# Kernel tuning notes

Hardware: AMD Instinct MI355X
Metric: run time of the kernel (lower is better)

Reference implementation:

```python
import jax, jax.numpy as jnp
import numpy as np

DIM = 256; HEADS = 8; DEPTH = 2; DFF = 128
T = 64      # timesteps (transformer batch dim for s_transformer)
N = 2048    # total agents
S = 256     # number of segments (scenes)
L = 8       # agents per segment (N = S*L)
HD = DIM // HEADS
LN_EPS = 1e-5


def _ln(x, w, b):
    m = x.mean(-1, keepdims=True)
    v = x.var(-1, keepdims=True)
    return (x - m) / jnp.sqrt(v + LN_EPS) * w + b


def _mha(x, qkvw, qkvb, ow, ob):
    B, Sq, D = x.shape
    qkv = x @ qkvw.T + qkvb                      # [B,Sq,3D]
    q, k, v = jnp.split(qkv, 3, axis=-1)
    def sp(t):
        return t.reshape(B, Sq, HEADS, HD).transpose(0, 2, 1, 3)
    q, k, v = sp(q), sp(k), sp(v)
    a = jax.nn.softmax(jnp.einsum('bhqd,bhkd->bhqk', q, k) * (1.0 / (HD ** 0.5)))
    o = jnp.einsum('bhqk,bhkd->bhqd', a, v).transpose(0, 2, 1, 3).reshape(B, Sq, D)
    return o @ ow.T + ob


def _layer(x, qkvw, qkvb, ow, ob, l1w, l1b, l2w, l2b, ln1w, ln1b, ln2w, ln2b):
    # PyTorch TransformerEncoderLayer, post-norm, relu FFN
    x = _ln(x + _mha(x, qkvw, qkvb, ow, ob), ln1w, ln1b)
    h = jax.nn.relu(x @ l1w.T + l1b) @ l2w.T + l2b
    return _ln(x + h, ln2w, ln2b)


def _encoder(x, qkvw, qkvb, ow, ob, l1w, l1b, l2w, l2b, ln1w, ln1b, ln2w, ln2b):
    for i in range(DEPTH):
        x = _layer(x, qkvw[i], qkvb[i], ow[i], ob[i], l1w[i], l1b[i],
                   l2w[i], l2b[i], ln1w[i], ln1b[i], ln2w[i], ln2b[i])
    return x


def setup_inputs() -> dict:
    key = jax.random.key(0)
    ks = iter(jax.random.split(key, 64))
    def rn(shape, scale=0.05):
        return jax.random.normal(next(ks), shape, dtype=jnp.float32) * scale
    inp = {}
    inp['moveinfo'] = jax.random.normal(next(ks), (N, T, 2), dtype=jnp.float32)
    starts = jnp.arange(S, dtype=jnp.int32) * L
    inp['seq_start_end'] = jnp.stack([starts, starts + L], axis=1)  # [S,2]
    inp['w_in'] = rn((DIM, 2)); inp['b_in'] = rn((DIM,))
    for p in ('s', 't'):
        inp[p + '_qkvw'] = rn((DEPTH, 3 * DIM, DIM)); inp[p + '_qkvb'] = rn((DEPTH, 3 * DIM))
        inp[p + '_ow'] = rn((DEPTH, DIM, DIM)); inp[p + '_ob'] = rn((DEPTH, DIM))
        inp[p + '_l1w'] = rn((DEPTH, DFF, DIM)); inp[p + '_l1b'] = rn((DEPTH, DFF))
        inp[p + '_l2w'] = rn((DEPTH, DIM, DFF)); inp[p + '_l2b'] = rn((DEPTH, DIM))
        inp[p + '_ln1w'] = jnp.ones((DEPTH, DIM)); inp[p + '_ln1b'] = jnp.zeros((DEPTH, DIM))
        inp[p + '_ln2w'] = jnp.ones((DEPTH, DIM)); inp[p + '_ln2b'] = jnp.zeros((DEPTH, DIM))
    return inp


def reference(moveinfo, seq_start_end, w_in, b_in,
              s_qkvw, s_qkvb, s_ow, s_ob, s_l1w, s_l1b, s_l2w, s_l2b,
              s_ln1w, s_ln1b, s_ln2w, s_ln2b,
              t_qkvw, t_qkvb, t_ow, t_ob, t_l1w, t_l1b, t_l2w, t_l2b,
              t_ln1w, t_ln1b, t_ln2w, t_ln2b):
    # to_dim: Linear(2, dim) + exact GELU
    s_in = jax.nn.gelu(jnp.einsum('ntc,dc->ntd', moveinfo, w_in) + b_in, approximate=False)
    s_in = s_in.transpose(1, 0, 2)                       # [T, N, D]
    # gather equal-length segments: ragged loop batched as one attention call
    idx = seq_start_end[:, 0][:, None] + jnp.arange(L)   # [S, L]
    seg = s_in[:, idx, :].reshape(T * S, L, DIM)         # [T*S, L, D]
    cls = jnp.full((T * S, 1, DIM), 1e-5, dtype=s_in.dtype)
    x = jnp.concatenate([cls, seg], axis=1)              # [T*S, 1+L, D]
    x = _encoder(x, s_qkvw, s_qkvb, s_ow, s_ob, s_l1w, s_l1b, s_l2w, s_l2b,
                 s_ln1w, s_ln1b, s_ln2w, s_ln2b)
    t_in = x[:, 0, :].reshape(T, S, DIM).transpose(1, 0, 2)  # [S, T, D]
    out = _encoder(t_in, t_qkvw, t_qkvb, t_ow, t_ob, t_l1w, t_l1b, t_l2w, t_l2b,
                   t_ln1w, t_ln1b, t_ln2w, t_ln2b)
    return out
```

## Files before the change

### kernel.cpp

```cpp
#include <hip/hip_runtime.h>
#include <hip/hip_bf16.h>
#include <math.h>

typedef __bf16 bf16_t;
typedef float floatx4 __attribute__((ext_vector_type(4)));
typedef bf16_t bf16x8 __attribute__((ext_vector_type(8)));

typedef __attribute__((address_space(1))) void g_void;
typedef __attribute__((address_space(3))) void lds_void;

__device__ __forceinline__ void ldg_lds16(const bf16_t* g, bf16_t* l) {
    __builtin_amdgcn_global_load_lds((g_void*)g, (lds_void*)l, 16, 0, 0);
}

__device__ __forceinline__ void unpack4(uint2 r, float* o) {
    o[0] = __uint_as_float((r.x & 0xffffu) << 16); o[1] = __uint_as_float(r.x & 0xffff0000u);
    o[2] = __uint_as_float((r.y & 0xffffu) << 16); o[3] = __uint_as_float(r.y & 0xffff0000u);
}

__global__ void cvt_weights(const float* __restrict__ sqkvw, const float* __restrict__ sow,
                            const float* __restrict__ sl1w,  const float* __restrict__ sl2w,
                            const float* __restrict__ tqkvw, const float* __restrict__ tow,
                            const float* __restrict__ tl1w,  const float* __restrict__ tl2w,
                            bf16_t* __restrict__ dst) {
    int i = blockIdx.x * 256 + threadIdx.x;
    float v;
    if      (i <  393216) v = sqkvw[i];
    else if (i <  524288) v = sow  [i -  393216];
    else if (i <  589824) v = sl1w [i -  524288];
    else if (i <  655360) v = sl2w [i -  589824];
    else if (i < 1048576) v = tqkvw[i -  655360];
    else if (i < 1179648) v = tow  [i - 1048576];
    else if (i < 1245184) v = tl1w [i - 1179648];
    else                  v = tl2w [i - 1245184];
    dst[i] = (bf16_t)v;
}

__global__ void embed_k(const float* __restrict__ mv, const float* __restrict__ w_in,
                        const float* __restrict__ b_in, bf16_t* __restrict__ x, int b0) {
    int blk = blockIdx.x; int d = threadIdx.x;
    int tok = blk % 9; int lb = blk / 9;
    size_t oidx = (size_t)blk * 256 + d;
    if (tok == 0) { x[oidx] = (bf16_t)1e-5f; return; }
    int bb = b0 + lb; int t = bb >> 8; int s = bb & 255;
    int n = s * 8 + (tok - 1);
    float m0 = mv[((size_t)n * 64 + t) * 2];
    float m1 = mv[((size_t)n * 64 + t) * 2 + 1];
    float v = m0 * w_in[2 * d] + m1 * w_in[2 * d + 1] + b_in[d];
    v = 0.5f * v * (1.0f + erff(v * 0.70710678118654752f));
    x[oidx] = (bf16_t)v;
}

__global__ __launch_bounds__(256) void gemm_bt(const bf16_t* __restrict__ A,
                                               const bf16_t* __restrict__ W,
                                               const float* __restrict__ bias,
                                               bf16_t* __restrict__ C,
                                               int M, int N, int K, int relu) {
    __shared__ __align__(16) bf16_t As[8192];
    __shared__ __align__(16) bf16_t Ws[8192];
    int MT = M >> 7, NT = N >> 7;
    int g = blockIdx.x;
    int m_t, n_t;
    if ((MT & 7) == 0) {
        int x = g & 7, q = g >> 3;
        m_t = (q / NT) * 8 + x;
        n_t = q % NT;
    } else {
        m_t = g / NT; n_t = g % NT;
    }
    int tid = threadIdx.x;
    int lane = tid & 63;
    int wave = tid >> 6;
    int m0 = m_t * 128;
    int n0 = n_t * 128;
    int wm = (wave & 1) * 64;
    int wn = (wave >> 1) * 64;
    int arow = tid >> 2;
    int acol = (tid & 3) * 8;
    int fm = lane & 15;
    int fq = lane >> 4;

    floatx4 acc[4][4] = {};

    const bf16_t* Ag = A + (size_t)(m0 + arow) * K + acol;
    const bf16_t* Wg = W + (size_t)(n0 + arow) * K + acol;

    for (int k0 = 0; k0 < K; k0 += 64) {
        __syncthreads();
        ldg_lds16(Ag + k0,                       &As[tid * 8]);
        ldg_lds16(Ag + k0 + (size_t)64 * K,      &As[2048 + tid * 8]);
        ldg_lds16(Ag + k0 + 32,                  &As[4096 + tid * 8]);
        ldg_lds16(Ag + k0 + 32 + (size_t)64 * K, &As[6144 + tid * 8]);
        ldg_lds16(Wg + k0,                       &Ws[tid * 8]);
        ldg_lds16(Wg + k0 + (size_t)64 * K,      &Ws[2048 + tid * 8]);
        ldg_lds16(Wg + k0 + 32,                  &Ws[4096 + tid * 8]);
        ldg_lds16(Wg + k0 + 32 + (size_t)64 * K, &Ws[6144 + tid * 8]);
        __syncthreads();

#pragma unroll
        for (int sl = 0; sl < 2; sl++) {
            int base = sl * 4096;
            bf16x8 af[4], wf[4];
#pragma unroll
            for (int mi = 0; mi < 4; mi++)
                af[mi] = *(const bf16x8*)&As[base + (wm + mi * 16 + fm) * 32 + fq * 8];
#pragma unroll
            for (int ni = 0; ni < 4; ni++)
                wf[ni] = *(const bf16x8*)&Ws[base + (wn + ni * 16 + fm) * 32 + fq * 8];
#pragma unroll
            for (int mi = 0; mi < 4; mi++)
#pragma unroll
                for (int ni = 0; ni < 4; ni++)
                    acc[mi][ni] = __builtin_amdgcn_mfma_f32_16x16x32_bf16(wf[ni], af[mi], acc[mi][ni], 0, 0, 0);
        }
    }

#pragma unroll
    for (int mi = 0; mi < 4; mi++) {
        int row = m0 + wm + mi * 16 + fm;
#pragma unroll
        for (int ni = 0; ni < 4; ni++) {
            int colb = n0 + wn + ni * 16 + fq * 4;
            float4 b4 = *(const float4*)(bias + colb);
            float v0 = acc[mi][ni][0] + b4.x;
            float v1 = acc[mi][ni][1] + b4.y;
            float v2 = acc[mi][ni][2] + b4.z;
            float v3 = acc[mi][ni][3] + b4.w;
            if (relu) {
                v0 = fmaxf(v0, 0.f); v1 = fmaxf(v1, 0.f);
                v2 = fmaxf(v2, 0.f); v3 = fmaxf(v3, 0.f);
            }
            bf16_t t4[4] = {(bf16_t)v0, (bf16_t)v1, (bf16_t)v2, (bf16_t)v3};
            *(uint2*)(C + (size_t)row * N + colb) = *(uint2*)t4;
        }
    }
}

__device__ __forceinline__ void epi_resln64(
    floatx4 (&acc)[4][4], int m0, int wn, int fm, int fq, int wave,
    const float* __restrict__ bias, const bf16_t* __restrict__ res_bf,
    const float* __restrict__ res_f, const float* __restrict__ lnw,
    const float* __restrict__ lnb, bf16_t* out_bf, float* out_f,
    bf16_t* cls_bf, float* cls_f, int b0,
    float (*rs)[64], float (*rss)[64]) {
    float s[4] = {0.f, 0.f, 0.f, 0.f}, ss[4] = {0.f, 0.f, 0.f, 0.f};
#pragma unroll
    for (int mi = 0; mi < 4; mi++) {
        size_t row = (size_t)(m0 + mi * 16 + fm);
#pragma unroll
        for (int ni = 0; ni < 4; ni++) {
            int col = wn + ni * 16 + fq * 4;
            float4 b4 = *(const float4*)(bias + col);
            float r4[4];
            if (res_f) {
                float4 t = *(const float4*)(res_f + row * 256 + col);
                r4[0] = t.x; r4[1] = t.y; r4[2] = t.z; r4[3] = t.w;
            } else {
                unpack4(*(const uint2*)(res_bf + row * 256 + col), r4);
            }
            float v0 = acc[mi][ni][0] + b4.x + r4[0];
            float v1 = acc[mi][ni][1] + b4.y + r4[1];
            float v2 = acc[mi][ni][2] + b4.z + r4[2];
            float v3 = acc[mi][ni][3] + b4.w + r4[3];
            acc[mi][ni][0] = v0; acc[mi][ni][1] = v1;
            acc[mi][ni][2] = v2; acc[mi][ni][3] = v3;
            s[mi] += v0 + v1 + v2 + v3;
            ss[mi] += v0 * v0 + v1 * v1 + v2 * v2 + v3 * v3;
        }
    }
#pragma unroll
    for (int mi = 0; mi < 4; mi++) {
        s[mi]  += __shfl_xor(s[mi], 16);  s[mi]  += __shfl_xor(s[mi], 32);
        ss[mi] += __shfl_xor(ss[mi], 16); ss[mi] += __shfl_xor(ss[mi], 32);
    }
    if (fq == 0) {
#pragma unroll
        for (int mi = 0; mi < 4; mi++) {
            rs [wave][mi * 16 + fm] = s[mi];
            rss[wave][mi * 16 + fm] = ss[mi];
        }
    }
    __syncthreads();
#pragma unroll
    for (int mi = 0; mi < 4; mi++) {
        int lrow = mi * 16 + fm;
        int grow = m0 + lrow;
        size_t row = (size_t)grow;
        float mean = (rs[0][lrow] + rs[1][lrow] + rs[2][lrow] + rs[3][lrow]) * (1.f / 256.f);
        float var  = (rss[0][lrow] + rss[1][lrow] + rss[2][lrow] + rss[3][lrow]) * (1.f / 256.f)
                   - mean * mean;
        float inv = rsqrtf(var + 1e-5f);
        int is_cls = (cls_bf != nullptr) && (grow % 9 == 0);
        size_t di = 0;
        if (is_cls) {
            int bb = b0 + grow / 9;
            int tt = bb >> 8, sseg = bb & 255;
            di = ((size_t)(sseg * 64 + tt)) * 256;
        }
#pragma unroll
        for (int ni = 0; ni < 4; ni++) {
            int col = wn + ni * 16 + fq * 4;
            float4 w4 = *(const float4*)(lnw + col);
            float4 bl = *(const float4*)(lnb + col);
            float o0 = (acc[mi][ni][0] - mean) * inv * w4.x + bl.x;
            float o1 = (acc[mi][ni][1] - mean) * inv * w4.y + bl.y;
            float o2 = (acc[mi][ni][2] - mean) * inv * w4.z + bl.z;
            float o3 = (acc[mi][ni][3] - mean) * inv * w4.w + bl.w;
            if (out_bf) {
                bf16_t t4[4] = {(bf16_t)o0, (bf16_t)o1, (bf16_t)o2, (bf16_t)o3};
                *(uint2*)(out_bf + row * 256 + col) = *(uint2*)t4;
            }
            if (out_f) {
                float4 t; t.x = o0; t.y = o1; t.z = o2; t.w = o3;
                *(float4*)(out_f + row * 256 + col) = t;
            }
            if (is_cls) {
                bf16_t t4[4] = {(bf16_t)o0, (bf16_t)o1, (bf16_t)o2, (bf16_t)o3};
                *(uint2*)(cls_bf + di + col) = *(uint2*)t4;
                float4 t; t.x = o0; t.y = o1; t.z = o2; t.w = o3;
                *(float4*)(cls_f + di + col) = t;
            }
        }
    }
}

__global__ __launch_bounds__(256) void proj_ffn_ln(const bf16_t* __restrict__ A,
                                                   const bf16_t* __restrict__ Wo,
                                                   const float* __restrict__ ob,
                                                   const bf16_t* __restrict__ res,
                                                   const float* __restrict__ ln1w,
                                                   const float* __restrict__ ln1b,
                                                   const bf16_t* __restrict__ w1,
                                                   const float* __restrict__ b1,
                                                   const bf16_t* __restrict__ w2,
                                                   const float* __restrict__ b2,
                                                   const float* __restrict__ ln2w,
                                                   const float* __restrict__ ln2b,
                                                   bf16_t* out_bf,
                                                   bf16_t* cls_bf, float* cls_f, int b0) {
    __shared__ __align__(16) bf16_t As[4096];
    __shared__ __align__(16) bf16_t Ws[16384];
    __shared__ __align__(16) bf16_t Xs[64 * 264];
    __shared__ float rs[4][64], rss[4][64];
    int tid = threadIdx.x, lane = tid & 63, wave = tid >> 6;
    int m0 = blockIdx.x * 64;
    int wn = wave * 64;
    int wn1 = wave * 32;
    int fm = lane & 15, fq = lane >> 4;

    floatx4 acc[4][4] = {};
    {
        const bf16_t* Ag = A + (size_t)(m0 + (tid >> 2)) * 256 + (tid & 3) * 8;
        const bf16_t* Wg = Wo + (size_t)(tid >> 2) * 256 + (tid & 3) * 8;
        auto STAGE = [&](int r, int b) {
            int k = r * 32;
            ldg_lds16(Ag + k, &As[b * 2048 + tid * 8]);
#pragma unroll
            for (int j = 0; j < 4; j++)
                ldg_lds16(Wg + k + j * 16384, &Ws[b * 8192 + j * 2048 + tid * 8]);
        };
        auto COMPUTE = [&](int b) {
            bf16x8 af[4], wf[4];
#pragma unroll
            for (int mi = 0; mi < 4; mi++)
                af[mi] = *(const bf16x8*)&As[b * 2048 + (mi * 16 + fm) * 32 + fq * 8];
#pragma unroll
            for (int ni = 0; ni < 4; ni++)
                wf[ni] = *(const bf16x8*)&Ws[b * 8192 + (wn + ni * 16 + fm) * 32 + fq * 8];
#pragma unroll
            for (int mi = 0; mi < 4; mi++)
#pragma unroll
                for (int ni = 0; ni < 4; ni++)
                    acc[mi][ni] = __builtin_amdgcn_mfma_f32_16x16x32_bf16(wf[ni], af[mi], acc[mi][ni], 0, 0, 0);
        };
        STAGE(0, 0);
        __syncthreads();
        for (int r = 0; r < 7; ++r) {
            STAGE(r + 1, (r + 1) & 1);
            COMPUTE(r & 1);
            __syncthreads();
        }
        COMPUTE(1);
    }

    {
        float s[4] = {0.f, 0.f, 0.f, 0.f}, ss[4] = {0.f, 0.f, 0.f, 0.f};
#pragma unroll
        for (int mi = 0; mi < 4; mi++) {
            size_t row = (size_t)(m0 + mi * 16 + fm);
#pragma unroll
            for (int ni = 0; ni < 4; ni++) {
                int col = wn + ni * 16 + fq * 4;
                float4 b4 = *(const float4*)(ob + col);
                float r4[4];
                unpack4(*(const uint2*)(res + row * 256 + col), r4);
                float v0 = acc[mi][ni][0] + b4.x + r4[0];
                float v1 = acc[mi][ni][1] + b4.y + r4[1];
                float v2 = acc[mi][ni][2] + b4.z + r4[2];
                float v3 = acc[mi][ni][3] + b4.w + r4[3];
                acc[mi][ni][0] = v0; acc[mi][ni][1] = v1;
                acc[mi][ni][2] = v2; acc[mi][ni][3] = v3;
                s[mi] += v0 + v1 + v2 + v3;
                ss[mi] += v0 * v0 + v1 * v1 + v2 * v2 + v3 * v3;
            }
        }
#pragma unroll
        for (int mi = 0; mi < 4; mi++) {
            s[mi]  += __shfl_xor(s[mi], 16);  s[mi]  += __shfl_xor(s[mi], 32);
            ss[mi] += __shfl_xor(ss[mi], 16); ss[mi] += __shfl_xor(ss[mi], 32);
        }
        if (fq == 0) {
#pragma unroll
            for (int mi = 0; mi < 4; mi++) {
                rs [wave][mi * 16 + fm] = s[mi];
                rss[wave][mi * 16 + fm] = ss[mi];
            }
        }
        __syncthreads();
#pragma unroll
        for (int mi = 0; mi < 4; mi++) {
            int lrow = mi * 16 + fm;
            float mean = (rs[0][lrow] + rs[1][lrow] + rs[2][lrow] + rs[3][lrow]) * (1.f / 256.f);
            float var  = (rss[0][lrow] + rss[1][lrow] + rss[2][lrow] + rss[3][lrow]) * (1.f / 256.f)
                       - mean * mean;
            float inv = rsqrtf(var + 1e-5f);
#pragma unroll
            for (int ni = 0; ni < 4; ni++) {
                int col = wn + ni * 16 + fq * 4;
                float4 w4 = *(const float4*)(ln1w + col);
                float4 bl = *(const float4*)(ln1b + col);
                bf16_t t4[4];
                t4[0] = (bf16_t)((acc[mi][ni][0] - mean) * inv * w4.x + bl.x);
                t4[1] = (bf16_t)((acc[mi][ni][1] - mean) * inv * w4.y + bl.y);
                t4[2] = (bf16_t)((acc[mi][ni][2] - mean) * inv * w4.z + bl.z);
                t4[3] = (bf16_t)((acc[mi][ni][3] - mean) * inv * w4.w + bl.w);
                *(uint2*)&Xs[lrow * 264 + col] = *(uint2*)t4;
            }
        }
    }
    __syncthreads();

    floatx4 acc1[4][2] = {};
#pragma unroll
    for (int ks = 0; ks < 8; ks++) {
        bf16x8 af[4];
#pragma unroll
        for (int mi = 0; mi < 4; mi++)
            af[mi] = *(const bf16x8*)&Xs[(mi * 16 + fm) * 264 + ks * 32 + fq * 8];
#pragma unroll
        for (int ni = 0; ni < 2; ni++) {
            bf16x8 wf = *(const bf16x8*)(w1 + (size_t)(wn1 + ni * 16 + fm) * 256 + ks * 32 + fq * 8);
#pragma unroll
            for (int mi = 0; mi < 4; mi++)
                acc1[mi][ni] = __builtin_amdgcn_mfma_f32_16x16x32_bf16(wf, af[mi], acc1[mi][ni], 0, 0, 0);
        }
    }
    bf16_t* Hs = Ws;
#pragma unroll
    for (int mi = 0; mi < 4; mi++) {
        int row = mi * 16 + fm;
#pragma unroll
        for (int ni = 0; ni < 2; ni++) {
            int c = wn1 + ni * 16 + fq * 4;
            float4 b4 = *(const float4*)(b1 + c);
            bf16_t t4[4];
            t4[0] = (bf16_t)fmaxf(acc1[mi][ni][0] + b4.x, 0.f);
            t4[1] = (bf16_t)fmaxf(acc1[mi][ni][1] + b4.y, 0.f);
            t4[2] = (bf16_t)fmaxf(acc1[mi][ni][2] + b4.z, 0.f);
            t4[3] = (bf16_t)fmaxf(acc1[mi][ni][3] + b4.w, 0.f);
            *(uint2*)&Hs[(c >> 5) * 2560 + row * 40 + (c & 31)] = *(uint2*)t4;
        }
    }
    __syncthreads();

    floatx4 acc2[4][4] = {};
#pragma unroll
    for (int ks = 0; ks < 4; ks++) {
        bf16x8 af2[4];
#pragma unroll
        for (int mi = 0; mi < 4; mi++)
            af2[mi] = *(const bf16x8*)&Hs[ks * 2560 + (mi * 16 + fm) * 40 + fq * 8];
#pragma unroll
        for (int ni = 0; ni < 4; ni++) {
            bf16x8 wf2 = *(const bf16x8*)(w2 + (size_t)(wn + ni * 16 + fm) * 128 + ks * 32 + fq * 8);
#pragma unroll
            for (int mi = 0; mi < 4; mi++)
                acc2[mi][ni] = __builtin_amdgcn_mfma_f32_16x16x32_bf16(wf2, af2[mi], acc2[mi][ni], 0, 0, 0);
        }
    }

    {
        float s[4] = {0.f, 0.f, 0.f, 0.f}, ss[4] = {0.f, 0.f, 0.f, 0.f};
#pragma unroll
        for (int mi = 0; mi < 4; mi++) {
            int lrow = mi * 16 + fm;
#pragma unroll
            for (int ni = 0; ni < 4; ni++) {
                int col = wn + ni * 16 + fq * 4;
                float4 b4 = *(const float4*)(b2 + col);
                float r4[4];
                unpack4(*(const uint2*)&Xs[lrow * 264 + col], r4);
                float v0 = acc2[mi][ni][0] + b4.x + r4[0];
                float v1 = acc2[mi][ni][1] + b4.y + r4[1];
                float v2 = acc2[mi][ni][2] + b4.z + r4[2];
                float v3 = acc2[mi][ni][3] + b4.w + r4[3];
                acc2[mi][ni][0] = v0; acc2[mi][ni][1] = v1;
                acc2[mi][ni][2] = v2; acc2[mi][ni][3] = v3;
                s[mi] += v0 + v1 + v2 + v3;
                ss[mi] += v0 * v0 + v1 * v1 + v2 * v2 + v3 * v3;
            }
        }
#pragma unroll
        for (int mi = 0; mi < 4; mi++) {
            s[mi]  += __shfl_xor(s[mi], 16);  s[mi]  += __shfl_xor(s[mi], 32);
            ss[mi] += __shfl_xor(ss[mi], 16); ss[mi] += __shfl_xor(ss[mi], 32);
        }
        __syncthreads();
        if (fq == 0) {
#pragma unroll
            for (int mi = 0; mi < 4; mi++) {
                rs [wave][mi * 16 + fm] = s[mi];
                rss[wave][mi * 16 + fm] = ss[mi];
            }
        }
        __syncthreads();
#pragma unroll
        for (int mi = 0; mi < 4; mi++) {
            int lrow = mi * 16 + fm;
            int grow = m0 + lrow;
            size_t row = (size_t)grow;
            float mean = (rs[0][lrow] + rs[1][lrow] + rs[2][lrow] + rs[3][lrow]) * (1.f / 256.f);
            float var  = (rss[0][lrow] + rss[1][lrow] + rss[2][lrow] + rss[3][lrow]) * (1.f / 256.f)
                       - mean * mean;
            float inv = rsqrtf(var + 1e-5f);
            int is_cls = (cls_bf != nullptr) && (grow % 9 == 0);
            size_t di = 0;
            if (is_cls) {
                int bb = b0 + grow / 9;
                int tt = bb >> 8, sseg = bb & 255;
                di = ((size_t)(sseg * 64 + tt)) * 256;
            }
#pragma unroll
            for (int ni = 0; ni < 4; ni++) {
                int col = wn + ni * 16 + fq * 4;
                float4 w4 = *(const float4*)(ln2w + col);
                float4 bl = *(const float4*)(ln2b + col);
                float o0 = (acc2[mi][ni][0] - mean) * inv * w4.x + bl.x;
                float o1 = (acc2[mi][ni][1] - mean) * inv * w4.y + bl.y;
                float o2 = (acc2[mi][ni][2] - mean) * inv * w4.z + bl.z;
                float o3 = (acc2[mi][ni][3] - mean) * inv * w4.w + bl.w;
                if (out_bf) {
                    bf16_t t4[4] = {(bf16_t)o0, (bf16_t)o1, (bf16_t)o2, (bf16_t)o3};
                    *(uint2*)(out_bf + row * 256 + col) = *(uint2*)t4;
                }
                if (is_cls) {
                    bf16_t t4[4] = {(bf16_t)o0, (bf16_t)o1, (bf16_t)o2, (bf16_t)o3};
                    *(uint2*)(cls_bf + di + col) = *(uint2*)t4;
                    float4 t; t.x = o0; t.y = o1; t.z = o2; t.w = o3;
                    *(float4*)(cls_f + di + col) = t;
                }
            }
        }
    }
}

__global__ __launch_bounds__(256) void gemm_proj_ln(const bf16_t* __restrict__ A,
                                                    const bf16_t* __restrict__ W,
                                                    const float* __restrict__ bias,
                                                    const bf16_t* __restrict__ res_bf,
                                                    const float* __restrict__ res_f,
                                                    const float* __restrict__ lnw,
                                                    const float* __restrict__ lnb,
                                                    bf16_t* out_bf,
                                                    float* out_f) {
    __shared__ __align__(16) bf16_t As[4096];
    __shared__ __align__(16) bf16_t Ws[16384];
    __shared__ float rs[4][64], rss[4][64];
    int tid = threadIdx.x;
    int lane = tid & 63, wave = tid >> 6;
    int m0 = blockIdx.x * 64;
    int wn = wave * 64;
    int fm = lane & 15, fq = lane >> 4;
    floatx4 acc[4][4] = {};
    const bf16_t* Ag = A + (size_t)(m0 + (tid >> 2)) * 256 + (tid & 3) * 8;
    const bf16_t* Wg = W + (size_t)(tid >> 2) * 256 + (tid & 3) * 8;

    auto STAGE = [&](int r, int b) {
        int k = r * 32;
        ldg_lds16(Ag + k, &As[b * 2048 + tid * 8]);
#pragma unroll
        for (int j = 0; j < 4; j++)
            ldg_lds16(Wg + k + j * 16384, &Ws[b * 8192 + j * 2048 + tid * 8]);
    };
    auto COMPUTE = [&](int b) {
        bf16x8 af[4], wf[4];
#pragma unroll
        for (int mi = 0; mi < 4; mi++)
            af[mi] = *(const bf16x8*)&As[b * 2048 + (mi * 16 + fm) * 32 + fq * 8];
#pragma unroll
        for (int ni = 0; ni < 4; ni++)
            wf[ni] = *(const bf16x8*)&Ws[b * 8192 + (wn + ni * 16 + fm) * 32 + fq * 8];
#pragma unroll
        for (int mi = 0; mi < 4; mi++)
#pragma unroll
            for (int ni = 0; ni < 4; ni++)
                acc[mi][ni] = __builtin_amdgcn_mfma_f32_16x16x32_bf16(wf[ni], af[mi], acc[mi][ni], 0, 0, 0);
    };

    STAGE(0, 0);
    __syncthreads();
    for (int r = 0; r < 7; ++r) {
        STAGE(r + 1, (r + 1) & 1);
        COMPUTE(r & 1);
        __syncthreads();
    }
    COMPUTE(1);
    epi_resln64(acc, m0, wn, fm, fq, wave, bias, res_bf, res_f, lnw, lnb,
                out_bf, out_f, nullptr, nullptr, 0, rs, rss);
}

__global__ __launch_bounds__(256) void gemm_ffn_ln(const bf16_t* __restrict__ X,
                                                   const bf16_t* __restrict__ w1,
                                                   const float* __restrict__ b1,
                                                   const bf16_t* __restrict__ w2,
                                                   const float* __restrict__ b2,
                                                   const float* __restrict__ lnw,
                                                   const float* __restrict__ lnb,
                                                   const float* __restrict__ res_f,
                                                   bf16_t* out_bf, float* out_f,
                                                   bf16_t* cls_bf, float* cls_f, int b0) {
    __shared__ __align__(16) bf16_t As[4096];
    __shared__ __align__(16) bf16_t Ws[8192];
    __shared__ __align__(16) bf16_t Hs[10240];
    __shared__ float rs[4][64], rss[4][64];
    int tid = threadIdx.x, lane = tid & 63, wave = tid >> 6;
    int m0 = blockIdx.x * 64;
    int wn1 = wave * 32;
    int wn2 = wave * 64;
    int fm = lane & 15, fq = lane >> 4;
    floatx4 acc[4][2] = {};
    const bf16_t* Ag = X + (size_t)(m0 + (tid >> 2)) * 256 + (tid & 3) * 8;
    const bf16_t* Wg = w1 + (size_t)(tid >> 2) * 256 + (tid & 3) * 8;

    auto STAGE = [&](int r, int b) {
        int k = r * 32;
        ldg_lds16(Ag + k, &As[b * 2048 + tid * 8]);
#pragma unroll
        for (int j = 0; j < 2; j++)
            ldg_lds16(Wg + k + j * 16384, &Ws[b * 4096 + j * 2048 + tid * 8]);
    };
    auto COMPUTE = [&](int b) {
        bf16x8 af[4], wf[2];
#pragma unroll
        for (int mi = 0; mi < 4; mi++)
            af[mi] = *(const bf16x8*)&As[b * 2048 + (mi * 16 + fm) * 32 + fq * 8];
#pragma unroll
        for (int ni = 0; ni < 2; ni++)
            wf[ni] = *(const bf16x8*)&Ws[b * 4096 + (wn1 + ni * 16 + fm) * 32 + fq * 8];
#pragma unroll
        for (int mi = 0; mi < 4; mi++)
#pragma unroll
            for (int ni = 0; ni < 2; ni++)
                acc[mi][ni] = __builtin_amdgcn_mfma_f32_16x16x32_bf16(wf[ni], af[mi], acc[mi][ni], 0, 0, 0);
    };

    STAGE(0, 0);
    __syncthreads();
    for (int r = 0; r < 7; ++r) {
        STAGE(r + 1, (r + 1) & 1);
        COMPUTE(r & 1);
        __syncthreads();
    }
    COMPUTE(1);

#pragma unroll
    for (int mi = 0; mi < 4; mi++) {
        int row = mi * 16 + fm;
#pragma unroll
        for (int ni = 0; ni < 2; ni++) {
            int c = wn1 + ni * 16 + fq * 4;
            float4 b4 = *(const float4*)(b1 + c);
            bf16_t t4[4];
            t4[0] = (bf16_t)fmaxf(acc[mi][ni][0] + b4.x, 0.f);
            t4[1] = (bf16_t)fmaxf(acc[mi][ni][1] + b4.y, 0.f);
            t4[2] = (bf16_t)fmaxf(acc[mi][ni][2] + b4.z, 0.f);
            t4[3] = (bf16_t)fmaxf(acc[mi][ni][3] + b4.w, 0.f);
            *(uint2*)&Hs[(c >> 5) * 2560 + row * 40 + (c & 31)] = *(uint2*)t4;
        }
    }
    __syncthreads();
    floatx4 acc2[4][4] = {};
#pragma unroll
    for (int ks = 0; ks < 4; ks++) {
        bf16x8 af2[4];
#pragma unroll
        for (int mi = 0; mi < 4; mi++)
            af2[mi] = *(const bf16x8*)&Hs[ks * 2560 + (mi * 16 + fm) * 40 + fq * 8];
#pragma unroll
        for (int ni = 0; ni < 4; ni++) {
            bf16x8 wf2 = *(const bf16x8*)(w2 + (size_t)(wn2 + ni * 16 + fm) * 128 + ks * 32 + fq * 8);
#pragma unroll
            for (int mi = 0; mi < 4; mi++)
                acc2[mi][ni] = __builtin_amdgcn_mfma_f32_16x16x32_bf16(wf2, af2[mi], acc2[mi][ni], 0, 0, 0);
        }
    }
    epi_resln64(acc2, m0, wn2, fm, fq, wave, b2, X, res_f, lnw, lnb,
                out_bf, out_f, cls_bf, cls_f, b0, rs, rss);
}

__global__ __launch_bounds__(320) void attn9_k(const bf16_t* __restrict__ qkv,
                                               bf16_t* __restrict__ ao) {
    __shared__ __align__(16) bf16_t kv[36 * 512];
    int b = blockIdx.x; int tid = threadIdx.x;
    const bf16_t* src = qkv + (size_t)b * 27648;
    for (int c = tid; c < 2304; c += 320) {
        int row = c >> 6; int off = (c & 63) << 3;
        *(uint4*)&kv[row * 512 + off] = *(const uint4*)&src[row * 768 + 256 + off];
    }
    __syncthreads();
    if (tid < 288) {
        int s = tid / 72; int rem = tid - s * 72; int h = rem / 9; int i = rem - h * 9;
        const bf16_t* qp = src + (size_t)(s * 9 + i) * 768 + h * 32;
        float qf[32];
#pragma unroll
        for (int c = 0; c < 4; c++) {
            bf16x8 t8 = *(const bf16x8*)(qp + c * 8);
#pragma unroll
            for (int e = 0; e < 8; e++) qf[c * 8 + e] = (float)t8[e];
        }
        float sc[9]; float mx = -1e30f;
#pragma unroll
        for (int j = 0; j < 9; j++) {
            const bf16_t* kp = &kv[(s * 9 + j) * 512 + h * 32];
            float d = 0.f;
#pragma unroll
            for (int c = 0; c < 4; c++) {
                bf16x8 t8 = *(const bf16x8*)(kp + c * 8);
#pragma unroll
                for (int e = 0; e < 8; e++) d += qf[c * 8 + e] * (float)t8[e];
            }
            d *= 0.17677669529663687f;
            sc[j] = d; mx = fmaxf(mx, d);
        }
        float den = 0.f;
#pragma unroll
        for (int j = 0; j < 9; j++) { sc[j] = __expf(sc[j] - mx); den += sc[j]; }
        float inv = 1.0f / den;
        float of[32] = {};
#pragma unroll
        for (int j = 0; j < 9; j++) {
            const bf16_t* vp = &kv[(s * 9 + j) * 512 + 256 + h * 32];
            float w = sc[j];
#pragma unroll
            for (int c = 0; c < 4; c++) {
                bf16x8 t8 = *(const bf16x8*)(vp + c * 8);
#pragma unroll
                for (int e = 0; e < 8; e++) of[c * 8 + e] += w * (float)t8[e];
            }
        }
        bf16_t* dst = ao + ((size_t)(b * 4 + s) * 9 + i) * 256 + h * 32;
#pragma unroll
        for (int c = 0; c < 4; c++) {
            bf16x8 o8;
#pragma unroll
            for (int e = 0; e < 8; e++) o8[e] = (bf16_t)(of[c * 8 + e] * inv);
            *(bf16x8*)(dst + c * 8) = o8;
        }
    }
}

__global__ __launch_bounds__(256) void attn64_k(const bf16_t* __restrict__ qkv,
                                                bf16_t* __restrict__ ao) {
    __shared__ __align__(16) float kk[64 * 36];
    __shared__ __align__(16) float vv[64 * 36];
    __shared__ __align__(16) float pp[64 * 64];
    __shared__ float mloc[4 * 64];
    __shared__ float sloc[4 * 64];
    int s = blockIdx.x >> 3, h = blockIdx.x & 7;
    int t = threadIdx.x;
    int i = t & 63;
    int wq = t >> 6;

    {
        int r = t >> 2, c = t & 3;
        const bf16_t* kb = qkv + ((size_t)(s * 64 + r)) * 768 + h * 32 + 256 + c * 8;
        bf16x8 k8 = *(const bf16x8*)kb;
        bf16x8 v8 = *(const bf16x8*)(kb + 256);
        float* kd = &kk[r * 36 + c * 8];
        float* vd = &vv[r * 36 + c * 8];
#pragma unroll
        for (int e = 0; e < 8; e++) { kd[e] = (float)k8[e]; vd[e] = (float)v8[e]; }
    }
    const bf16_t* qb = qkv + ((size_t)(s * 64 + i)) * 768 + h * 32;
    float qf[32];
#pragma unroll
    for (int c = 0; c < 4; c++) {
        bf16x8 t8 = *(const bf16x8*)(qb + c * 8);
#pragma unroll
        for (int e = 0; e < 8; e++) qf[c * 8 + e] = (float)t8[e];
    }
    __syncthreads();

    float sc[16]; float mx = -1e30f;
#pragma unroll
    for (int jj = 0; jj < 16; jj++) {
        int j = wq * 16 + jj;
        const float* kr = &kk[j * 36];
        float d = 0.f;
#pragma unroll
        for (int c = 0; c < 8; c++) {
            float4 k4 = *(const float4*)(kr + c * 4);
            d += qf[c*4+0]*k4.x + qf[c*4+1]*k4.y + qf[c*4+2]*k4.z + qf[c*4+3]*k4.w;
        }
        d *= 0.17677669529663687f;
        sc[jj] = d; mx = fmaxf(mx, d);
    }
    float se = 0.f;
#pragma unroll
    for (int jj = 0; jj < 16; jj++) se += __expf(sc[jj] - mx);
    mloc[wq * 64 + i] = mx;
    sloc[wq * 64 + i] = se;
    __syncthreads();

    float m0 = mloc[i], m1 = mloc[64 + i], m2 = mloc[128 + i], m3 = mloc[192 + i];
    float gm = fmaxf(fmaxf(m0, m1), fmaxf(m2, m3));
    float D = sloc[i] * __expf(m0 - gm) + sloc[64 + i] * __expf(m1 - gm)
            + sloc[128 + i] * __expf(m2 - gm) + sloc[192 + i] * __expf(m3 - gm);

#pragma unroll
    for (int jj = 0; jj < 16; jj++)
        pp[(wq * 16 + jj) * 64 + i] = __expf(sc[jj] - gm);
    __syncthreads();

    float of[8] = {};
    for (int j = 0; j < 64; j++) {
        float w = pp[j * 64 + i];
        const float* vr = &vv[j * 36 + wq * 8];
        float4 va = *(const float4*)vr;
        float4 vb = *(const float4*)(vr + 4);
        of[0] += w * va.x; of[1] += w * va.y; of[2] += w * va.z; of[3] += w * va.w;
        of[4] += w * vb.x; of[5] += w * vb.y; of[6] += w * vb.z; of[7] += w * vb.w;
    }
    float invD = 1.0f / D;
    bf16_t o8[8];
#pragma unroll
    for (int e = 0; e < 8; e++) o8[e] = (bf16_t)(of[e] * invD);
    *(uint4*)(ao + ((size_t)(s * 64 + i)) * 256 + h * 32 + wq * 8) = *(uint4*)o8;
}

extern "C" void kernel_launch(void* const* d_in, const int* in_sizes, int n_in,
                              void* d_out, int out_size, void* d_ws, size_t ws_size,
                              hipStream_t stream) {
    const float* mv   = (const float*)d_in[0];
    const float* w_in = (const float*)d_in[2];
    const float* b_in = (const float*)d_in[3];
    const float* sp[12]; const float* tp[12];
    for (int i = 0; i < 12; i++) { sp[i] = (const float*)d_in[4 + i]; tp[i] = (const float*)d_in[16 + i]; }

    bf16_t* wbf = (bf16_t*)d_ws;
    bf16_t* txb = wbf + 1310720;
    float*  txf = (float*)(txb + 4194304);
    bf16_t* pool = (bf16_t*)(txf + 4194304);

    long long headB = 2621440LL + 8388608LL + 16777216LL;
    long long cand[5] = {16384, 8192, 4096, 2048, 1024};
    int BC = 1024;
    for (int c = 0; c < 5; c++) {
        long long poolB = cand[c] * 11520LL * 2;
        if (poolB < 33554432LL) poolB = 33554432LL;
        if ((size_t)(headB + poolB) <= ws_size) { BC = (int)cand[c]; break; }
    }

    cvt_weights<<<5120, 256, 0, stream>>>(sp[0], sp[2], sp[4], sp[6], tp[0], tp[2], tp[4], tp[6], wbf);

    const int M = BC * 9;
    const int MT64 = M / 64;
    bf16_t* xc    = pool;
    bf16_t* qkvb_ = pool + (long long)BC * 2304;
    bf16_t* aob   = qkvb_ + (long long)BC * 6912;

    for (int b0 = 0; b0 < 16384; b0 += BC) {
        embed_k<<<dim3(M), 256, 0, stream>>>(mv, w_in, b_in, xc, b0);
        for (int l = 0; l < 2; l++) {
            const bf16_t* wq = wbf + 0      + l * 196608;
            const bf16_t* wo = wbf + 393216 + l * 65536;
            const bf16_t* w1 = wbf + 524288 + l * 32768;
            const bf16_t* w2 = wbf + 589824 + l * 32768;
            gemm_bt<<<dim3((M / 128) * 6), 256, 0, stream>>>(xc, wq, sp[1] + l * 768, qkvb_, M, 768, 256, 0);
            attn9_k<<<dim3(BC / 4), 320, 0, stream>>>(qkvb_, aob);
            proj_ffn_ln<<<dim3(MT64), 256, 0, stream>>>(aob, wo, sp[3] + l * 256,
                                                        xc, sp[8] + l * 256, sp[9] + l * 256,
                                                        w1, sp[5] + l * 128,
                                                        w2, sp[7] + l * 256,
                                                        sp[10] + l * 256, sp[11] + l * 256,
                                                        (l == 0) ? xc : (bf16_t*)nullptr,
                                                        (l == 0) ? (bf16_t*)nullptr : txb,
                                                        (l == 0) ? (float*)nullptr : txf, b0);
        }
    }

    bf16_t* tqkv = pool;
    bf16_t* tao  = pool + 12582912;
    for (int l = 0; l < 2; l++) {
        gemm_bt<<<dim3(128 * 6), 256, 0, stream>>>(txb, wbf + 655360 + l * 196608, tp[1] + l * 768,
                                                   tqkv, 16384, 768, 256, 0);
        attn64_k<<<dim3(2048), 256, 0, stream>>>(tqkv, tao);
        gemm_proj_ln<<<dim3(256), 256, 0, stream>>>(tao, wbf + 1048576 + l * 65536, tp[3] + l * 256,
                                                    (const bf16_t*)nullptr, txf,
                                                    tp[8] + l * 256, tp[9] + l * 256,
                                                    txb, txf);
        gemm_ffn_ln<<<dim3(256), 256, 0, stream>>>(txb, wbf + 1179648 + l * 32768, tp[5] + l * 128,
                                                   wbf + 1245184 + l * 32768, tp[7] + l * 256,
                                                   tp[10] + l * 256, tp[11] + l * 256,
                                                   txf,
                                                   (l == 0) ? txb : (bf16_t*)nullptr,
                                                   (l == 0) ? txf : (float*)d_out,
                                                   (bf16_t*)nullptr, (float*)nullptr, 0);
    }
}
```

Measured before the change: 969.4 us.

## Shrink LDS in proj_ffn_ln by loading A once and reading Wo from global

The fused out-projection, FFN and LayerNorm kernel no longer double-buffers A and Wo tiles through LDS. It loads the 64x256 A tile into Xs once, reads Wo fragments straight from global (L2-cached) memory, and reuses a single smaller buffer for the hidden activations and the reduction scratch, with padded strides. LDS use per block drops from about 76KB to about 52KB, which may let more blocks share a CU. In exchange, weight reads go through global memory with no async staging or overlap, and an extra barrier is needed because the scratch buffer is shared with the hidden activations.

```diff
diff --git a/kernel.cpp b/kernel.cpp
--- a/kernel.cpp
+++ b/kernel.cpp
@@ -238,50 +238,43 @@
                                                    const float* __restrict__ ln2b,
                                                    bf16_t* out_bf,
                                                    bf16_t* cls_bf, float* cls_f, int b0) {
-    __shared__ __align__(16) bf16_t As[4096];
-    __shared__ __align__(16) bf16_t Ws[16384];
-    __shared__ __align__(16) bf16_t Xs[64 * 264];
-    __shared__ float rs[4][64], rss[4][64];
+    __shared__ __align__(16) bf16_t Xs[64 * 268];
+    __shared__ __align__(16) bf16_t HsU[9216];
+    float* rsp  = (float*)HsU;
+    float* rssp = rsp + 256;
     int tid = threadIdx.x, lane = tid & 63, wave = tid >> 6;
     int m0 = blockIdx.x * 64;
     int wn = wave * 64;
     int wn1 = wave * 32;
     int fm = lane & 15, fq = lane >> 4;
 
+    {
+        int r0 = tid >> 5, c0 = (tid & 31) * 8;
+        const bf16_t* Ag = A + (size_t)(m0 + r0) * 256 + c0;
+#pragma unroll
+        for (int it = 0; it < 8; it++) {
+            bf16x8 v = *(const bf16x8*)(Ag + (size_t)it * 8 * 256);
+            *(bf16x8*)&Xs[(it * 8 + r0) * 268 + c0] = v;
+        }
+    }
+    __syncthreads();
+
     floatx4 acc[4][4] = {};
-    {
-        const bf16_t* Ag = A + (size_t)(m0 + (tid >> 2)) * 256 + (tid & 3) * 8;
-        const bf16_t* Wg = Wo + (size_t)(tid >> 2) * 256 + (tid & 3) * 8;
-        auto STAGE = [&](int r, int b) {
-            int k = r * 32;
-            ldg_lds16(Ag + k, &As[b * 2048 + tid * 8]);
-#pragma unroll
-            for (int j = 0; j < 4; j++)
-                ldg_lds16(Wg + k + j * 16384, &Ws[b * 8192 + j * 2048 + tid * 8]);
-        };
-        auto COMPUTE = [&](int b) {
-            bf16x8 af[4], wf[4];
+#pragma unroll
+    for (int ks = 0; ks < 8; ks++) {
+        bf16x8 af[4];
+#pragma unroll
+        for (int mi = 0; mi < 4; mi++)
+            af[mi] = *(const bf16x8*)&Xs[(mi * 16 + fm) * 268 + ks * 32 + fq * 8];
+#pragma unroll
+        for (int ni = 0; ni < 4; ni++) {
+            bf16x8 wf = *(const bf16x8*)(Wo + (size_t)(wn + ni * 16 + fm) * 256 + ks * 32 + fq * 8);
 #pragma unroll
             for (int mi = 0; mi < 4; mi++)
-                af[mi] = *(const bf16x8*)&As[b * 2048 + (mi * 16 + fm) * 32 + fq * 8];
-#pragma unroll
-            for (int ni = 0; ni < 4; ni++)
-                wf[ni] = *(const bf16x8*)&Ws[b * 8192 + (wn + ni * 16 + fm) * 32 + fq * 8];
-#pragma unroll
-            for (int mi = 0; mi < 4; mi++)
-#pragma unroll
-                for (int ni = 0; ni < 4; ni++)
-                    acc[mi][ni] = __builtin_amdgcn_mfma_f32_16x16x32_bf16(wf[ni], af[mi], acc[mi][ni], 0, 0, 0);
-        };
-        STAGE(0, 0);
-        __syncthreads();
-        for (int r = 0; r < 7; ++r) {
-            STAGE(r + 1, (r + 1) & 1);
-            COMPUTE(r & 1);
-            __syncthreads();
-        }
-        COMPUTE(1);
-    }
+                acc[mi][ni] = __builtin_amdgcn_mfma_f32_16x16x32_bf16(wf, af[mi], acc[mi][ni], 0, 0, 0);
+        }
+    }
+    __syncthreads();
 
     {
         float s[4] = {0.f, 0.f, 0.f, 0.f}, ss[4] = {0.f, 0.f, 0.f, 0.f};
@@ -312,16 +305,16 @@
         if (fq == 0) {
 #pragma unroll
             for (int mi = 0; mi < 4; mi++) {
-                rs [wave][mi * 16 + fm] = s[mi];
-                rss[wave][mi * 16 + fm] = ss[mi];
+                rsp [wave * 64 + mi * 16 + fm] = s[mi];
+                rssp[wave * 64 + mi * 16 + fm] = ss[mi];
             }
         }
         __syncthreads();
 #pragma unroll
         for (int mi = 0; mi < 4; mi++) {
             int lrow = mi * 16 + fm;
-            float mean = (rs[0][lrow] + rs[1][lrow] + rs[2][lrow] + rs[3][lrow]) * (1.f / 256.f);
-            float var  = (rss[0][lrow] + rss[1][lrow] + rss[2][lrow] + rss[3][lrow]) * (1.f / 256.f)
+            float mean = (rsp[lrow] + rsp[64 + lrow] + rsp[128 + lrow] + rsp[192 + lrow]) * (1.f / 256.f);
+            float var  = (rssp[lrow] + rssp[64 + lrow] + rssp[128 + lrow] + rssp[192 + lrow]) * (1.f / 256.f)
                        - mean * mean;
             float inv = rsqrtf(var + 1e-5f);
 #pragma unroll
@@ -334,7 +327,7 @@
                 t4[1] = (bf16_t)((acc[mi][ni][1] - mean) * inv * w4.y + bl.y);
                 t4[2] = (bf16_t)((acc[mi][ni][2] - mean) * inv * w4.z + bl.z);
                 t4[3] = (bf16_t)((acc[mi][ni][3] - mean) * inv * w4.w + bl.w);
-                *(uint2*)&Xs[lrow * 264 + col] = *(uint2*)t4;
+                *(uint2*)&Xs[lrow * 268 + col] = *(uint2*)t4;
             }
         }
     }
@@ -346,7 +339,7 @@
         bf16x8 af[4];
 #pragma unroll
         for (int mi = 0; mi < 4; mi++)
-            af[mi] = *(const bf16x8*)&Xs[(mi * 16 + fm) * 264 + ks * 32 + fq * 8];
+            af[mi] = *(const bf16x8*)&Xs[(mi * 16 + fm) * 268 + ks * 32 + fq * 8];
 #pragma unroll
         for (int ni = 0; ni < 2; ni++) {
             bf16x8 wf = *(const bf16x8*)(w1 + (size_t)(wn1 + ni * 16 + fm) * 256 + ks * 32 + fq * 8);
@@ -355,7 +348,6 @@
                 acc1[mi][ni] = __builtin_amdgcn_mfma_f32_16x16x32_bf16(wf, af[mi], acc1[mi][ni], 0, 0, 0);
         }
     }
-    bf16_t* Hs = Ws;
 #pragma unroll
     for (int mi = 0; mi < 4; mi++) {
         int row = mi * 16 + fm;
@@ -368,7 +360,7 @@
             t4[1] = (bf16_t)fmaxf(acc1[mi][ni][1] + b4.y, 0.f);
             t4[2] = (bf16_t)fmaxf(acc1[mi][ni][2] + b4.z, 0.f);
             t4[3] = (bf16_t)fmaxf(acc1[mi][ni][3] + b4.w, 0.f);
-            *(uint2*)&Hs[(c >> 5) * 2560 + row * 40 + (c & 31)] = *(uint2*)t4;
+            *(uint2*)&HsU[(c >> 5) * 2304 + row * 36 + (c & 31)] = *(uint2*)t4;
         }
     }
     __syncthreads();
@@ -379,7 +371,7 @@
         bf16x8 af2[4];
 #pragma unroll
         for (int mi = 0; mi < 4; mi++)
-            af2[mi] = *(const bf16x8*)&Hs[ks * 2560 + (mi * 16 + fm) * 40 + fq * 8];
+            af2[mi] = *(const bf16x8*)&HsU[ks * 2304 + (mi * 16 + fm) * 36 + fq * 8];
 #pragma unroll
         for (int ni = 0; ni < 4; ni++) {
             bf16x8 wf2 = *(const bf16x8*)(w2 + (size_t)(wn + ni * 16 + fm) * 128 + ks * 32 + fq * 8);
@@ -388,6 +380,7 @@
                 acc2[mi][ni] = __builtin_amdgcn_mfma_f32_16x16x32_bf16(wf2, af2[mi], acc2[mi][ni], 0, 0, 0);
         }
     }
+    __syncthreads();
 
     {
         float s[4] = {0.f, 0.f, 0.f, 0.f}, ss[4] = {0.f, 0.f, 0.f, 0.f};
@@ -399,7 +392,7 @@
                 int col = wn + ni * 16 + fq * 4;
                 float4 b4 = *(const float4*)(b2 + col);
                 float r4[4];
-                unpack4(*(const uint2*)&Xs[lrow * 264 + col], r4);
+                unpack4(*(const uint2*)&Xs[lrow * 268 + col], r4);
                 float v0 = acc2[mi][ni][0] + b4.x + r4[0];
                 float v1 = acc2[mi][ni][1] + b4.y + r4[1];
                 float v2 = acc2[mi][ni][2] + b4.z + r4[2];
@@ -415,12 +408,11 @@
             s[mi]  += __shfl_xor(s[mi], 16);  s[mi]  += __shfl_xor(s[mi], 32);
             ss[mi] += __shfl_xor(ss[mi], 16); ss[mi] += __shfl_xor(ss[mi], 32);
         }
-        __syncthreads();
         if (fq == 0) {
 #pragma unroll
             for (int mi = 0; mi < 4; mi++) {
-                rs [wave][mi * 16 + fm] = s[mi];
-                rss[wave][mi * 16 + fm] = ss[mi];
+                rsp [wave * 64 + mi * 16 + fm] = s[mi];
+                rssp[wave * 64 + mi * 16 + fm] = ss[mi];
             }
         }
         __syncthreads();
@@ -429,8 +421,8 @@
             int lrow = mi * 16 + fm;
             int grow = m0 + lrow;
             size_t row = (size_t)grow;
-            float mean = (rs[0][lrow] + rs[1][lrow] + rs[2][lrow] + rs[3][lrow]) * (1.f / 256.f);
-            float var  = (rss[0][lrow] + rss[1][lrow] + rss[2][lrow] + rss[3][lrow]) * (1.f / 256.f)
+            float mean = (rsp[lrow] + rsp[64 + lrow] + rsp[128 + lrow] + rsp[192 + lrow]) * (1.f / 256.f);
+            float var  = (rssp[lrow] + rssp[64 + lrow] + rssp[128 + lrow] + rssp[192 + lrow]) * (1.f / 256.f)
                        - mean * mean;
             float inv = rsqrtf(var + 1e-5f);
             int is_cls = (cls_bf != nullptr) && (grow % 9 == 0);
```

New measurement: 988.5 us. No clear change (+2.0%).
